# Kernel tuning notes

Measured on AMD Instinct MI355X. Metric: run time of the kernel, lower is better.

Reference implementation:

```python
import jax, jax.numpy as jnp
import numpy as np

NEG_INF = -1e30  # stand-in for -inf that is safe under fp16/bf16 softmax


def setup_inputs() -> dict:
    key = jax.random.key(0)
    k1, k2, k3, k4 = jax.random.split(key, 4)
    B, T, C, H = 4, 4096, 1024, 64
    x = jax.random.normal(k1, (B, T, C), dtype=jnp.float32)
    Wq = jax.random.normal(k2, (C, H), dtype=jnp.float32) * (C ** -0.5)
    Wk = jax.random.normal(k3, (C, H), dtype=jnp.float32) * (C ** -0.5)
    Wv = jax.random.normal(k4, (C, H), dtype=jnp.float32) * (C ** -0.5)
    return {"x": x, "Wq": Wq, "Wk": Wk, "Wv": Wv}


def reference(x, Wq, Wk, Wv):
    # x: [B,T,C]; Wq/Wk/Wv: [C,H]
    q = jnp.einsum('btc,ch->bth', x, Wq)
    k = jnp.einsum('btc,ch->bth', x, Wk)
    v = jnp.einsum('btc,ch->bth', x, Wv)
    # NOTE: original module applies NO 1/sqrt(head_size) scaling — faithful here.
    wei = jnp.einsum('bqh,bkh->bqk', q, k)  # [B,T,T]
    T = x.shape[1]
    causal = jnp.tril(jnp.ones((T, T), dtype=bool))
    wei = jnp.where(causal, wei, NEG_INF)
    wei = jax.nn.softmax(wei, axis=-1)
    # dropout: eval-mode identity
    out = jnp.einsum('bqk,bkh->bqh', wei, v)  # [B,T,H]
    return out
```

## Files before the change

### kernel.cpp

```cpp
#include <hip/hip_runtime.h>
#include <hip/hip_fp16.h>


typedef __attribute__((ext_vector_type(8))) short bf16x8;
typedef __attribute__((ext_vector_type(8))) unsigned short u16x8;
typedef __attribute__((ext_vector_type(4))) float f32x4;

__device__ __forceinline__ unsigned short f2bf(float f) {
  unsigned u = __float_as_uint(f);
  u += 0x7fffu + ((u >> 16) & 1u);
  return (unsigned short)(u >> 16);
}
__device__ __forceinline__ float bf2f(unsigned short s) {
  return __uint_as_float(((unsigned)s) << 16);
}
__device__ __forceinline__ unsigned cvt_pk_bf16(float lo, float hi) {
  unsigned r;
  asm("v_cvt_pk_bf16_f32 %0, %1, %2" : "=v"(r) : "v"(lo), "v"(hi));
  return r;
}
__device__ __forceinline__ void gload_lds16(const void* g, void* l) {
  __builtin_amdgcn_global_load_lds(
      (const __attribute__((address_space(1))) unsigned int*)g,
      (__attribute__((address_space(3))) unsigned int*)l, 16, 0, 0);
}
#define KSWZ(row, colb) ((((row) * 128) + (colb)) ^ (((row) & 7) << 4))

__global__ __launch_bounds__(256) void wsplit_kernel(
    const float* __restrict__ Wq, const float* __restrict__ Wk,
    const float* __restrict__ Wv,
    unsigned short* __restrict__ Wth, unsigned short* __restrict__ Wtl) {
  const int fl = blockIdx.x * 256 + threadIdx.x;
  const int lane = fl & 63;
  const int rest = fl >> 6;
  const int nf = rest % 12;
  const int ksq = rest / 12;
  const int n = nf * 16 + (lane & 15);
  const int k0 = ksq * 32 + (lane >> 4) * 8;
  const float* wp = (n < 64) ? Wq : ((n < 128) ? Wk : Wv);
  const int h = n & 63;
  u16x8 hi, lo;
#pragma unroll
  for (int j = 0; j < 8; ++j) {
    float v = wp[(size_t)(k0 + j) * 64 + h];
    unsigned short hh = f2bf(v);
    hi[j] = hh;
    lo[j] = f2bf(v - bf2f(hh));
  }
  const size_t base = (size_t)fl * 8;
  *reinterpret_cast<u16x8*>(&Wth[base]) = hi;
  *reinterpret_cast<u16x8*>(&Wtl[base]) = lo;
}

__global__ __launch_bounds__(256) void proj_mfma_kernel(
    const float* __restrict__ x,
    const unsigned short* __restrict__ Wth, const unsigned short* __restrict__ Wtl,
    unsigned short* __restrict__ qh, unsigned short* __restrict__ ql,
    unsigned short* __restrict__ kh, unsigned short* __restrict__ kl,
    unsigned short* __restrict__ vt) {
  __shared__ unsigned short Ah[2][32][72];
  __shared__ unsigned short Al[2][32][72];
  const int tid = threadIdx.x;
  const int w = tid >> 6;
  const int lane = tid & 63;
  const int l16 = lane & 15;
  const int g = lane >> 4;
  const int row0 = blockIdx.x * 32;
  const int sr = tid >> 3;
  const int sc = (tid & 7) * 8;

  f32x4 acc[2][3];
#pragma unroll
  for (int m = 0; m < 2; ++m)
#pragma unroll
    for (int f = 0; f < 3; ++f) {
      f32x4 z = {0.f, 0.f, 0.f, 0.f};
      acc[m][f] = z;
    }

  const size_t xrow = (size_t)(row0 + sr) * 1024 + sc;
  {
    const float4 xa = *reinterpret_cast<const float4*>(&x[xrow]);
    const float4 xb = *reinterpret_cast<const float4*>(&x[xrow + 4]);
    float v[8] = {xa.x, xa.y, xa.z, xa.w, xb.x, xb.y, xb.z, xb.w};
    u16x8 hv, lv;
#pragma unroll
    for (int j = 0; j < 8; ++j) {
      unsigned short hh = f2bf(v[j]);
      hv[j] = hh;
      lv[j] = f2bf(v[j] - bf2f(hh));
    }
    *reinterpret_cast<u16x8*>(&Ah[0][sr][sc]) = hv;
    *reinterpret_cast<u16x8*>(&Al[0][sr][sc]) = lv;
  }

  for (int step = 0; step < 16; ++step) {
    __syncthreads();
    float4 na, nb;
    if (step < 15) {
      na = *reinterpret_cast<const float4*>(&x[xrow + (size_t)(step + 1) * 64]);
      nb = *reinterpret_cast<const float4*>(&x[xrow + (size_t)(step + 1) * 64 + 4]);
    }
    const int cur = step & 1;
#pragma unroll
    for (int ks = 0; ks < 2; ++ks) {
      bf16x8 bh[3], bl[3];
#pragma unroll
      for (int f = 0; f < 3; ++f) {
        const size_t off = ((size_t)(step * 2 + ks) * 12 + (w * 3 + f)) * 512 + lane * 8;
        bh[f] = *reinterpret_cast<const bf16x8*>(&Wth[off]);
        bl[f] = *reinterpret_cast<const bf16x8*>(&Wtl[off]);
      }
      bf16x8 ah[2], al[2];
#pragma unroll
      for (int m = 0; m < 2; ++m) {
        const int ro = m * 16 + l16;
        const int co = ks * 32 + g * 8;
        ah[m] = *reinterpret_cast<const bf16x8*>(&Ah[cur][ro][co]);
        al[m] = *reinterpret_cast<const bf16x8*>(&Al[cur][ro][co]);
      }
#pragma unroll
      for (int m = 0; m < 2; ++m)
#pragma unroll
        for (int f = 0; f < 3; ++f) {
          acc[m][f] = __builtin_amdgcn_mfma_f32_16x16x32_bf16(ah[m], bh[f], acc[m][f], 0, 0, 0);
          acc[m][f] = __builtin_amdgcn_mfma_f32_16x16x32_bf16(ah[m], bl[f], acc[m][f], 0, 0, 0);
          acc[m][f] = __builtin_amdgcn_mfma_f32_16x16x32_bf16(al[m], bh[f], acc[m][f], 0, 0, 0);
        }
    }
    if (step < 15) {
      float v[8] = {na.x, na.y, na.z, na.w, nb.x, nb.y, nb.z, nb.w};
      u16x8 hv, lv;
#pragma unroll
      for (int j = 0; j < 8; ++j) {
        unsigned short hh = f2bf(v[j]);
        hv[j] = hh;
        lv[j] = f2bf(v[j] - bf2f(hh));
      }
      *reinterpret_cast<u16x8*>(&Ah[cur ^ 1][sr][sc]) = hv;
      *reinterpret_cast<u16x8*>(&Al[cur ^ 1][sr][sc]) = lv;
    }
  }

  const int b = row0 >> 12;
  const int tbase = row0 & 4095;
#pragma unroll
  for (int m = 0; m < 2; ++m)
#pragma unroll
    for (int f = 0; f < 3; ++f) {
      const int nn = w * 48 + f * 16;
      if (nn < 64) {
        const int h = nn + l16;
#pragma unroll
        for (int j = 0; j < 4; ++j) {
          const int row = row0 + m * 16 + 4 * g + j;
          const float val = acc[m][f][j];
          const unsigned short hi = f2bf(val);
          qh[(size_t)row * 64 + h] = hi;
          ql[(size_t)row * 64 + h] = f2bf(val - bf2f(hi));
        }
      } else if (nn < 128) {
        const int h = nn - 64 + l16;
#pragma unroll
        for (int j = 0; j < 4; ++j) {
          const int row = row0 + m * 16 + 4 * g + j;
          const float val = acc[m][f][j];
          const unsigned short hi = f2bf(val);
          kh[(size_t)row * 64 + h] = hi;
          kl[(size_t)row * 64 + h] = f2bf(val - bf2f(hi));
        }
      } else {
        const int h = nn - 128 + l16;
        ushort4 pv;
        pv.x = f2bf(acc[m][f][0]);
        pv.y = f2bf(acc[m][f][1]);
        pv.z = f2bf(acc[m][f][2]);
        pv.w = f2bf(acc[m][f][3]);
        const size_t a = ((size_t)b * 64 + h) * 4096 + tbase + m * 16 + 4 * g;
        *reinterpret_cast<ushort4*>(&vt[a]) = pv;
      }
    }
}

template <int PT, int NU_B>
__global__ __launch_bounds__(256) void attn_part_block_kernel(
    const unsigned short* __restrict__ qh, const unsigned short* __restrict__ ql,
    const unsigned short* __restrict__ kh, const unsigned short* __restrict__ kl,
    const unsigned short* __restrict__ vt,
    __half* __restrict__ OP, float* __restrict__ ML) {
  __shared__ __align__(16) unsigned short Khs[4096];
  __shared__ __align__(16) unsigned short Kls[4096];
  __shared__ __align__(16) unsigned short Vs[4096];
  __shared__ __align__(16) unsigned short pbuf[4][2][16][88];
  const int tid = threadIdx.x;
  const int w = tid >> 6;
  const int lane = tid & 63;
  const int l16 = lane & 15;
  const int g = lane >> 4;

  const int bx = blockIdx.x;
  const int xc = bx & 7;
  const int b = xc >> 1;
  const int s = 2 * (bx >> 3) + (xc & 1);
  int k = 0, pref = 0;
  for (;;) {
    const int np = (2 * k + 2 + PT - 1) / PT;
    if (s < pref + np) break;
    pref += np;
    ++k;
  }
  const int j4 = k;
  const int p = s - pref;
  const int ntiles = 2 * j4 + 2;
  const int t0 = p * PT;
  const int t1 = min(ntiles, t0 + PT);
  const int q0 = j4 * 128 + w * 32;
  const size_t rowbase = (size_t)b * 4096;

  bf16x8 q0hf[2], q0lf[2], q1hf[2], q1lf[2];
#pragma unroll
  for (int ss = 0; ss < 2; ++ss) {
    size_t a0 = (rowbase + q0 + l16) * 64 + ss * 32 + g * 8;
    q0hf[ss] = *reinterpret_cast<const bf16x8*>(&qh[a0]);
    q0lf[ss] = *reinterpret_cast<const bf16x8*>(&ql[a0]);
    size_t a1 = a0 + 16 * 64;
    q1hf[ss] = *reinterpret_cast<const bf16x8*>(&qh[a1]);
    q1lf[ss] = *reinterpret_cast<const bf16x8*>(&ql[a1]);
  }

  f32x4 o0[4], o1[4];
#pragma unroll
  for (int hb = 0; hb < 4; ++hb) {
    f32x4 z = {0.f, 0.f, 0.f, 0.f};
    o0[hb] = z;
    o1[hb] = z;
  }
  float m0 = -1e30f, l0 = 0.f, m1 = -1e30f, l1 = 0.f;

  for (int t = t0; t < t1; ++t) {
    const int kv0 = t * 64;
#pragma unroll
    for (int half = 0; half < 2; ++half) {
      const int te = half * 256 + w * 64 + lane;
      const int r = te >> 3;
      const int c8 = (te & 7) ^ (r & 7);
      const int ldsoff = half * 4096 + w * 1024 + lane * 16;
      gload_lds16(&kh[(rowbase + kv0 + r) * 64 + c8 * 8], (char*)Khs + ldsoff);
      gload_lds16(&kl[(rowbase + kv0 + r) * 64 + c8 * 8], (char*)Kls + ldsoff);
      gload_lds16(&vt[((size_t)b * 64 + r) * 4096 + kv0 + c8 * 8], (char*)Vs + ldsoff);
    }
    __syncthreads();

    f32x4 s0[4], s1[4];
#pragma unroll
    for (int kb = 0; kb < 4; ++kb) {
      bf16x8 khf[2], klf[2];
#pragma unroll
      for (int ss = 0; ss < 2; ++ss) {
        const int row = kb * 16 + l16;
        const int colb = ss * 64 + g * 16;
        khf[ss] = *reinterpret_cast<const bf16x8*>((const char*)Khs + KSWZ(row, colb));
        klf[ss] = *reinterpret_cast<const bf16x8*>((const char*)Kls + KSWZ(row, colb));
      }
      f32x4 a0 = {0.f, 0.f, 0.f, 0.f};
      f32x4 a1 = {0.f, 0.f, 0.f, 0.f};
#pragma unroll
      for (int ss = 0; ss < 2; ++ss) {
        a0 = __builtin_amdgcn_mfma_f32_16x16x32_bf16(khf[ss], q0hf[ss], a0, 0, 0, 0);
        a0 = __builtin_amdgcn_mfma_f32_16x16x32_bf16(khf[ss], q0lf[ss], a0, 0, 0, 0);
        a0 = __builtin_amdgcn_mfma_f32_16x16x32_bf16(klf[ss], q0hf[ss], a0, 0, 0, 0);
        a1 = __builtin_amdgcn_mfma_f32_16x16x32_bf16(khf[ss], q1hf[ss], a1, 0, 0, 0);
        a1 = __builtin_amdgcn_mfma_f32_16x16x32_bf16(khf[ss], q1lf[ss], a1, 0, 0, 0);
        a1 = __builtin_amdgcn_mfma_f32_16x16x32_bf16(klf[ss], q1hf[ss], a1, 0, 0, 0);
      }
      s0[kb] = a0;
      s1[kb] = a1;
    }
    bf16x8 vf[2][4];
#pragma unroll
    for (int ks = 0; ks < 2; ++ks)
#pragma unroll
      for (int hb = 0; hb < 4; ++hb) {
        const int row = hb * 16 + l16;
        const int colb = ks * 64 + g * 16;
        vf[ks][hb] = *reinterpret_cast<const bf16x8*>((const char*)Vs + KSWZ(row, colb));
      }
    if (kv0 + 63 > q0) {
#pragma unroll
      for (int kb = 0; kb < 4; ++kb)
#pragma unroll
        for (int jj = 0; jj < 4; ++jj) {
          const int kvg = kv0 + kb * 16 + 4 * g + jj;
          if (kvg > q0 + l16) s0[kb][jj] = -1e30f;
          if (kvg > q0 + 16 + l16) s1[kb][jj] = -1e30f;
        }
    }
    float rm0 = s0[0][0], rm1 = s1[0][0];
#pragma unroll
    for (int kb = 0; kb < 4; ++kb) {
      float c0 = fmaxf(fmaxf(s0[kb][0], s0[kb][1]), fmaxf(s0[kb][2], s0[kb][3]));
      float c1 = fmaxf(fmaxf(s1[kb][0], s1[kb][1]), fmaxf(s1[kb][2], s1[kb][3]));
      rm0 = fmaxf(rm0, c0);
      rm1 = fmaxf(rm1, c1);
    }
    rm0 = fmaxf(rm0, __shfl_xor(rm0, 16));
    rm0 = fmaxf(rm0, __shfl_xor(rm0, 32));
    rm1 = fmaxf(rm1, __shfl_xor(rm1, 16));
    rm1 = fmaxf(rm1, __shfl_xor(rm1, 32));
    const bool r0 = !__all(rm0 - m0 <= 8.f);
    const bool r1 = !__all(rm1 - m1 <= 8.f);
    const float mu0 = r0 ? fmaxf(m0, rm0) : m0;
    const float mu1 = r1 ? fmaxf(m1, rm1) : m1;
    const float al0 = r0 ? __expf(m0 - mu0) : 1.f;
    const float al1 = r1 ? __expf(m1 - mu1) : 1.f;
    float ps0 = 0.f, ps1 = 0.f;
#pragma unroll
    for (int kb = 0; kb < 4; ++kb)
#pragma unroll
      for (int jj = 0; jj < 4; ++jj) {
        const float e0 = __expf(s0[kb][jj] - mu0);
        const float e1 = __expf(s1[kb][jj] - mu1);
        s0[kb][jj] = e0;
        s1[kb][jj] = e1;
        ps0 += e0;
        ps1 += e1;
      }
    ps0 += __shfl_xor(ps0, 16);
    ps0 += __shfl_xor(ps0, 32);
    ps1 += __shfl_xor(ps1, 16);
    ps1 += __shfl_xor(ps1, 32);
    l0 = l0 * al0 + ps0;
    m0 = mu0;
    l1 = l1 * al1 + ps1;
    m1 = mu1;
#pragma unroll
    for (int kb = 0; kb < 4; ++kb) {
      *reinterpret_cast<unsigned*>(&pbuf[w][0][l16][kb * 16 + 4 * g]) =
          cvt_pk_bf16(s0[kb][0], s0[kb][1]);
      *reinterpret_cast<unsigned*>(&pbuf[w][0][l16][kb * 16 + 4 * g + 2]) =
          cvt_pk_bf16(s0[kb][2], s0[kb][3]);
      *reinterpret_cast<unsigned*>(&pbuf[w][1][l16][kb * 16 + 4 * g]) =
          cvt_pk_bf16(s1[kb][0], s1[kb][1]);
      *reinterpret_cast<unsigned*>(&pbuf[w][1][l16][kb * 16 + 4 * g + 2]) =
          cvt_pk_bf16(s1[kb][2], s1[kb][3]);
    }
    if (r0) {
#pragma unroll
      for (int jj = 0; jj < 4; ++jj) {
        const float a0r = __shfl(al0, 4 * g + jj);
#pragma unroll
        for (int hb = 0; hb < 4; ++hb) o0[hb][jj] *= a0r;
      }
    }
    if (r1) {
#pragma unroll
      for (int jj = 0; jj < 4; ++jj) {
        const float a1r = __shfl(al1, 4 * g + jj);
#pragma unroll
        for (int hb = 0; hb < 4; ++hb) o1[hb][jj] *= a1r;
      }
    }
    asm volatile("s_waitcnt lgkmcnt(0)" ::: "memory");
#pragma unroll
    for (int ks = 0; ks < 2; ++ks) {
      bf16x8 pa0 = *reinterpret_cast<const bf16x8*>(&pbuf[w][0][l16][ks * 32 + g * 8]);
      bf16x8 pa1 = *reinterpret_cast<const bf16x8*>(&pbuf[w][1][l16][ks * 32 + g * 8]);
#pragma unroll
      for (int hb = 0; hb < 4; ++hb) {
        o0[hb] = __builtin_amdgcn_mfma_f32_16x16x32_bf16(pa0, vf[ks][hb], o0[hb], 0, 0, 0);
        o1[hb] = __builtin_amdgcn_mfma_f32_16x16x32_bf16(pa1, vf[ks][hb], o1[hb], 0, 0, 0);
      }
    }
    __syncthreads();
  }

  const size_t u = (size_t)b * NU_B + s;
  __half* op = OP + u * 8192 + (size_t)w * 32 * 64;
#pragma unroll
  for (int jj = 0; jj < 4; ++jj) {
    const int srcr = 4 * g + jj;
    const float l0r = __shfl(l0, srcr);
    const float l1r = __shfl(l1, srcr);
#pragma unroll
    for (int hb = 0; hb < 4; ++hb) {
      op[(4 * g + jj) * 64 + hb * 16 + l16] = __float2half(o0[hb][jj] / l0r);
      op[(16 + 4 * g + jj) * 64 + hb * 16 + l16] = __float2half(o1[hb][jj] / l1r);
    }
  }
  float* ml = ML + u * 256 + w * 64;
  if (lane < 16) {
    ml[lane] = m0;
    ml[32 + lane] = l0;
  } else if (lane < 32) {
    ml[lane] = m1;
    ml[32 + lane] = l1;
  }
}

template <int PT, int NU_B>
__global__ __launch_bounds__(256) void attn_combine_kernel(
    const __half* __restrict__ OP, const float* __restrict__ ML,
    float* __restrict__ out) {
  const int tid = threadIdx.x;
  const int w = tid >> 6;
  const int lane = tid & 63;
  const int rid = blockIdx.x * 4 + w;
  const int b = rid >> 12;
  const int rr = rid & 4095;
  const int j4 = rr >> 7;
  const int local = rr & 127;
  const int nparts = (2 * j4 + 2 + PT - 1) / PT;
  int prefix = 0;
  for (int k = 0; k < j4; ++k) prefix += (2 * k + 2 + PT - 1) / PT;
  const size_t base = (size_t)b * NU_B + prefix;
  const int wv = local >> 5;
  const int tile = (local >> 4) & 1;
  const int rowin = local & 15;
  const int mi = wv * 64 + tile * 16 + rowin;

  float M = -1e30f;
  for (int p = 0; p < nparts; ++p) M = fmaxf(M, ML[(base + p) * 256 + mi]);
  float wsum = 0.f, acc = 0.f;
  for (int p = 0; p < nparts; ++p) {
    const float m = ML[(base + p) * 256 + mi];
    const float l = ML[(base + p) * 256 + 32 + mi];
    const float wg = l * __expf(m - M);
    wsum += wg;
    acc += wg * __half2float(OP[(base + p) * 8192 + (size_t)local * 64 + lane]);
  }
  out[(size_t)rid * 64 + lane] = acc / wsum;
}

extern "C" void kernel_launch(void* const* d_in, const int* in_sizes, int n_in,
                              void* d_out, int out_size, void* d_ws, size_t ws_size,
                              hipStream_t stream) {
  const float* x  = (const float*)d_in[0];
  const float* Wq = (const float*)d_in[1];
  const float* Wk = (const float*)d_in[2];
  const float* Wv = (const float*)d_in[3];
  float* out = (float*)d_out;

  const size_t N = (size_t)4 * 4096 * 64;
  const size_t WN = (size_t)192 * 1024;
  unsigned short* qh = (unsigned short*)d_ws;
  unsigned short* ql = qh + N;
  unsigned short* kh = ql + N;
  unsigned short* kl = kh + N;
  unsigned short* vt = kl + N;
  unsigned short* Wth = vt + N;
  unsigned short* Wtl = Wth + WN;
  __half* OP = (__half*)(Wtl + WN);
  const size_t base_need = (5 * N + 2 * WN) * 2;

  const size_t NU4 = 4 * 272, NU8 = 4 * 144;
  const size_t need4 = base_need + NU4 * 8192 * 2 + NU4 * 256 * 4;
  const size_t need8 = base_need + NU8 * 8192 * 2 + NU8 * 256 * 4;

  wsplit_kernel<<<dim3(96), dim3(256), 0, stream>>>(Wq, Wk, Wv, Wth, Wtl);
  proj_mfma_kernel<<<dim3(512), dim3(256), 0, stream>>>(x, Wth, Wtl, qh, ql, kh, kl, vt);
  if (ws_size >= need4) {
    float* ML = (float*)(OP + NU4 * 8192);
    attn_part_block_kernel<4, 272><<<dim3(NU4), dim3(256), 0, stream>>>(qh, ql, kh, kl, vt, OP, ML);
    attn_combine_kernel<4, 272><<<dim3(4096), dim3(256), 0, stream>>>(OP, ML, out);
  } else {
    float* ML = (float*)(OP + NU8 * 8192);
    attn_part_block_kernel<8, 144><<<dim3(NU8), dim3(256), 0, stream>>>(qh, ql, kh, kl, vt, OP, ML);
    attn_combine_kernel<8, 144><<<dim3(4096), dim3(256), 0, stream>>>(OP, ML, out);
  }
}
```

Measured before the change: 96.64 us.

## Prefetch projection weights one step ahead and x two steps ahead

In the QKV projection kernel, the bf16 hi/lo weight fragments for the next K-step are now loaded into registers one step ahead, and x tiles two steps ahead, using alternating register sets. The fp32-to-bf16 hi/lo split now uses the packed v_cvt_pk_bf16_f32 instruction instead of scalar rounding. The aim is to hide global-load latency behind the MFMA work and cut ALU work in the conversion. The trade-off is higher register pressure from holding two sets of weight fragments, which may reduce occupancy.

```diff
diff --git a/kernel.cpp b/kernel.cpp
--- a/kernel.cpp
+++ b/kernel.cpp
@@ -50,6 +50,24 @@
   const size_t base = (size_t)fl * 8;
   *reinterpret_cast<u16x8*>(&Wth[base]) = hi;
   *reinterpret_cast<u16x8*>(&Wtl[base]) = lo;
+}
+
+__device__ __forceinline__ void cvt_store8(unsigned short* dh, unsigned short* dl,
+                                           const float4& a, const float4& b) {
+  float v[8] = {a.x, a.y, a.z, a.w, b.x, b.y, b.z, b.w};
+  uint4 hp, lp;
+  unsigned* hpp = reinterpret_cast<unsigned*>(&hp);
+  unsigned* lpp = reinterpret_cast<unsigned*>(&lp);
+#pragma unroll
+  for (int p = 0; p < 4; ++p) {
+    const unsigned h = cvt_pk_bf16(v[2 * p], v[2 * p + 1]);
+    hpp[p] = h;
+    const float h0 = __uint_as_float(h << 16);
+    const float h1 = __uint_as_float(h & 0xffff0000u);
+    lpp[p] = cvt_pk_bf16(v[2 * p] - h0, v[2 * p + 1] - h1);
+  }
+  *reinterpret_cast<uint4*>(dh) = hp;
+  *reinterpret_cast<uint4*>(dl) = lp;
 }
 
 __global__ __launch_bounds__(256) void proj_mfma_kernel(
@@ -78,39 +96,52 @@
       acc[m][f] = z;
     }
 
-  const size_t xrow = (size_t)(row0 + sr) * 1024 + sc;
-  {
-    const float4 xa = *reinterpret_cast<const float4*>(&x[xrow]);
-    const float4 xb = *reinterpret_cast<const float4*>(&x[xrow + 4]);
-    float v[8] = {xa.x, xa.y, xa.z, xa.w, xb.x, xb.y, xb.z, xb.w};
-    u16x8 hv, lv;
-#pragma unroll
-    for (int j = 0; j < 8; ++j) {
-      unsigned short hh = f2bf(v[j]);
-      hv[j] = hh;
-      lv[j] = f2bf(v[j] - bf2f(hh));
-    }
-    *reinterpret_cast<u16x8*>(&Ah[0][sr][sc]) = hv;
-    *reinterpret_cast<u16x8*>(&Al[0][sr][sc]) = lv;
-  }
-
+  const float* xp = &x[(size_t)(row0 + sr) * 1024 + sc];
+
+  float4 x0a = *reinterpret_cast<const float4*>(xp);
+  float4 x0b = *reinterpret_cast<const float4*>(xp + 4);
+  float4 x1a = *reinterpret_cast<const float4*>(xp + 64);
+  float4 x1b = *reinterpret_cast<const float4*>(xp + 68);
+  cvt_store8(&Ah[0][sr][sc], &Al[0][sr][sc], x0a, x0b);
+
+  bf16x8 bhc[2][3], blc[2][3];
+#pragma unroll
+  for (int ks = 0; ks < 2; ++ks)
+#pragma unroll
+    for (int f = 0; f < 3; ++f) {
+      const size_t off = ((size_t)ks * 12 + (w * 3 + f)) * 512 + lane * 8;
+      bhc[ks][f] = *reinterpret_cast<const bf16x8*>(&Wth[off]);
+      blc[ks][f] = *reinterpret_cast<const bf16x8*>(&Wtl[off]);
+    }
+
+#pragma unroll 2
   for (int step = 0; step < 16; ++step) {
     __syncthreads();
-    float4 na, nb;
+    bf16x8 bhn[2][3], bln[2][3];
     if (step < 15) {
-      na = *reinterpret_cast<const float4*>(&x[xrow + (size_t)(step + 1) * 64]);
-      nb = *reinterpret_cast<const float4*>(&x[xrow + (size_t)(step + 1) * 64 + 4]);
+#pragma unroll
+      for (int ks = 0; ks < 2; ++ks)
+#pragma unroll
+        for (int f = 0; f < 3; ++f) {
+          const size_t off =
+              ((size_t)((step + 1) * 2 + ks) * 12 + (w * 3 + f)) * 512 + lane * 8;
+          bhn[ks][f] = *reinterpret_cast<const bf16x8*>(&Wth[off]);
+          bln[ks][f] = *reinterpret_cast<const bf16x8*>(&Wtl[off]);
+        }
+    }
+    if (step < 14) {
+      const float* px = xp + (size_t)(step + 2) * 64;
+      if ((step & 1) == 0) {
+        x0a = *reinterpret_cast<const float4*>(px);
+        x0b = *reinterpret_cast<const float4*>(px + 4);
+      } else {
+        x1a = *reinterpret_cast<const float4*>(px);
+        x1b = *reinterpret_cast<const float4*>(px + 4);
+      }
     }
     const int cur = step & 1;
 #pragma unroll
     for (int ks = 0; ks < 2; ++ks) {
-      bf16x8 bh[3], bl[3];
-#pragma unroll
-      for (int f = 0; f < 3; ++f) {
-        const size_t off = ((size_t)(step * 2 + ks) * 12 + (w * 3 + f)) * 512 + lane * 8;
-        bh[f] = *reinterpret_cast<const bf16x8*>(&Wth[off]);
-        bl[f] = *reinterpret_cast<const bf16x8*>(&Wtl[off]);
-      }
       bf16x8 ah[2], al[2];
 #pragma unroll
       for (int m = 0; m < 2; ++m) {
@@ -123,23 +154,24 @@
       for (int m = 0; m < 2; ++m)
 #pragma unroll
         for (int f = 0; f < 3; ++f) {
-          acc[m][f] = __builtin_amdgcn_mfma_f32_16x16x32_bf16(ah[m], bh[f], acc[m][f], 0, 0, 0);
-          acc[m][f] = __builtin_amdgcn_mfma_f32_16x16x32_bf16(ah[m], bl[f], acc[m][f], 0, 0, 0);
-          acc[m][f] = __builtin_amdgcn_mfma_f32_16x16x32_bf16(al[m], bh[f], acc[m][f], 0, 0, 0);
+          acc[m][f] = __builtin_amdgcn_mfma_f32_16x16x32_bf16(ah[m], bhc[ks][f], acc[m][f], 0, 0, 0);
+          acc[m][f] = __builtin_amdgcn_mfma_f32_16x16x32_bf16(ah[m], blc[ks][f], acc[m][f], 0, 0, 0);
+          acc[m][f] = __builtin_amdgcn_mfma_f32_16x16x32_bf16(al[m], bhc[ks][f], acc[m][f], 0, 0, 0);
         }
     }
     if (step < 15) {
-      float v[8] = {na.x, na.y, na.z, na.w, nb.x, nb.y, nb.z, nb.w};
-      u16x8 hv, lv;
-#pragma unroll
-      for (int j = 0; j < 8; ++j) {
-        unsigned short hh = f2bf(v[j]);
-        hv[j] = hh;
-        lv[j] = f2bf(v[j] - bf2f(hh));
-      }
-      *reinterpret_cast<u16x8*>(&Ah[cur ^ 1][sr][sc]) = hv;
-      *reinterpret_cast<u16x8*>(&Al[cur ^ 1][sr][sc]) = lv;
-    }
+      if (((step + 1) & 1) == 0)
+        cvt_store8(&Ah[cur ^ 1][sr][sc], &Al[cur ^ 1][sr][sc], x0a, x0b);
+      else
+        cvt_store8(&Ah[cur ^ 1][sr][sc], &Al[cur ^ 1][sr][sc], x1a, x1b);
+    }
+#pragma unroll
+    for (int ks = 0; ks < 2; ++ks)
+#pragma unroll
+      for (int f = 0; f < 3; ++f) {
+        bhc[ks][f] = bhn[ks][f];
+        blc[ks][f] = bln[ks][f];
+      }
   }
 
   const int b = row0 >> 12;
```

Measured after the change: 92.85 us. 3.9% less time.
